# Optimization experiments

Measured on AMD Instinct MI355X. Metric: run time of the kernel, lower is better.

The kernel has to match this reference:

```python
import jax, jax.numpy as jnp
import numpy as np

DIM = 256   # feat channels (init dim)
K = 32      # top-k neighbors (init k)
EPS = 1e-12 # torch F.normalize eps


def setup_inputs() -> dict:
    key = jax.random.key(0)
    # channels = DIM feat + 64 pos-encoding channels
    feat_pos = jax.random.normal(key, (16, 320, 32, 32), dtype=jnp.float32)
    return {"feat_pos": feat_pos}


def reference(feat_pos):
    b, ct, h, w = feat_pos.shape
    n = h * w
    # (b, c_total, h, w) -> (b, n, c_total)
    x = feat_pos.reshape(b, ct, n).transpose(0, 2, 1)
    feat = x[:, :, :DIM]          # (b, n, c)
    pos = x[:, :, DIM:]           # (b, n, p)
    # L2-normalize pos (torch F.normalize semantics: divide by max(norm, eps))
    pos = pos / jnp.maximum(jnp.linalg.norm(pos, axis=-1, keepdims=True), EPS)
    # pairwise cosine similarity (b, n, n)
    sim = jnp.einsum('bnd,bmd->bnm', pos, pos)
    # top-k neighbors per token (sorted descending, same as torch.topk)
    topksim, topkid = jax.lax.top_k(sim, K)          # (b, n, k)
    bidx = jnp.arange(b)[:, None, None]
    topkfeat = feat[bidx, topkid]                    # (b, n, k, c)
    attn = jax.nn.softmax(topksim, axis=-1)          # (b, n, k)
    out = jnp.einsum('bnk,bnkc->bnc', attn, topkfeat)  # (b, n, c)
    return out.reshape(b, h, w, DIM).transpose(0, 3, 1, 2)  # (b, c, h, w)
```

## Files before the change

kernel.cpp:

```cpp
#include <hip/hip_runtime.h>
#include <math.h>

#define CT    320
#define NPTS  1024
#define DFEAT 256
#define DPOS  64
#define KSEL  32

__global__ void gnn_rnj(const float* __restrict__ in, float* __restrict__ rnjg) {
  const int b     = blockIdx.x;
  const int batch = b >> 2;
  const int j     = ((b & 3) << 8) + threadIdx.x;
  const float* __restrict__ pbase = in + (size_t)batch * CT * NPTS + (size_t)DFEAT * NPTS;
  float s = 0.f;
#pragma unroll 8
  for (int d = 0; d < DPOS; ++d) {
    const float x = pbase[(size_t)d * NPTS + j];
    s = fmaf(x, x, s);
  }
  rnjg[batch * NPTS + j] = 1.0f / fmaxf(sqrtf(s), 1e-12f);
}

#define AROWS 16
#define DCH   2
#define QSTEP 6.103515625e-05f
__global__ __launch_bounds__(256, 4) void gnn_sim_topk(const float* __restrict__ in,
                                                       const float* __restrict__ rnjg,
                                                       float2* __restrict__ pairs) {
  __shared__ float pi[DPOS * 20];
  __shared__ float rnjL[NPTS];
  __shared__ float jt[3][DCH * 1024];
  __shared__ float cand[AROWS][68];

  const int p     = blockIdx.x;
  const int batch = ((p & 7) << 1) | ((p >> 3) & 1);
  const int chunk = p >> 4;
  const int i0    = chunk * AROWS;
  const int tid   = threadIdx.x;
  const int w     = tid >> 6;
  const int lane  = tid & 63;

  const float* __restrict__ pbase = in + (size_t)batch * CT * NPTS + (size_t)DFEAT * NPTS;

  {
    const int i = tid & 15;
    const int d0 = tid >> 4;
#pragma unroll
    for (int pass = 0; pass < 4; ++pass) {
      const int d = pass * 16 + d0;
      pi[d * 20 + i] = pbase[(size_t)d * NPTS + i0 + i];
    }
  }
  *(float4*)&rnjL[tid * 4] = *(const float4*)&rnjg[batch * NPTS + tid * 4];

#define JSTAGE(buf, c)                                                           \
  do {                                                                           \
    const int dd_   = (w >> 1);                                                  \
    const int half_ = (w & 1);                                                   \
    const float* src_ = pbase + (size_t)((c) * DCH + dd_) * NPTS + half_ * 512 + lane * 4; \
    float* dst_ = &jt[buf][dd_ * 1024 + half_ * 512];                            \
    __builtin_amdgcn_global_load_lds(                                            \
        (const __attribute__((address_space(1))) void*)(src_),                   \
        (__attribute__((address_space(3))) void*)(dst_), 16, 0, 0);              \
    __builtin_amdgcn_global_load_lds(                                            \
        (const __attribute__((address_space(1))) void*)(src_ + 256),             \
        (__attribute__((address_space(3))) void*)(dst_ + 256), 16, 0, 0);        \
  } while (0)

  JSTAGE(0, 0);
  JSTAGE(1, 1);
  asm volatile("s_waitcnt vmcnt(2)" ::: "memory");
  __syncthreads();

  float acc[4][16];
#pragma unroll
  for (int r = 0; r < 4; ++r)
#pragma unroll
    for (int s = 0; s < 16; ++s) acc[r][s] = 0.f;

  int cur = 0;
  for (int c = 0; c < DPOS / DCH; ++c) {
#pragma unroll
    for (int dd = 0; dd < DCH; ++dd) {
      const int d = c * DCH + dd;
      const float4 pv4 = *(const float4*)&pi[d * 20 + w * 4];
      const float pr_[4] = {pv4.x, pv4.y, pv4.z, pv4.w};
      float4 jv[4];
#pragma unroll
      for (int u = 0; u < 4; ++u)
        jv[u] = *(const float4*)&jt[cur][dd * 1024 + u * 256 + lane * 4];
#pragma unroll
      for (int r = 0; r < 4; ++r) {
#pragma unroll
        for (int u = 0; u < 4; ++u) {
          acc[r][u*4+0] = fmaf(pr_[r], jv[u].x, acc[r][u*4+0]);
          acc[r][u*4+1] = fmaf(pr_[r], jv[u].y, acc[r][u*4+1]);
          acc[r][u*4+2] = fmaf(pr_[r], jv[u].z, acc[r][u*4+2]);
          acc[r][u*4+3] = fmaf(pr_[r], jv[u].w, acc[r][u*4+3]);
        }
      }
    }
    if (c < DPOS / DCH - 2) {
      const int nbuf = (cur + 2 >= 3) ? cur - 1 : cur + 2;
      JSTAGE(nbuf, c + 2);
      asm volatile("s_waitcnt vmcnt(2)" ::: "memory");
    } else {
      asm volatile("s_waitcnt vmcnt(0)" ::: "memory");
    }
    __syncthreads();
    cur = (cur + 1 >= 3) ? 0 : cur + 1;
  }
#undef JSTAGE

  float4 rv[4];
#pragma unroll
  for (int u = 0; u < 4; ++u) rv[u] = *(const float4*)&rnjL[u * 256 + lane * 4];

#pragma unroll
  for (int r = 0; r < 4; ++r) {
    const int rglob = w * 4 + r;
    const float sc = rnjL[i0 + rglob];
    float v[16];
#pragma unroll
    for (int u = 0; u < 4; ++u) {
      v[u*4+0] = acc[r][u*4+0] * rv[u].x * sc;
      v[u*4+1] = acc[r][u*4+1] * rv[u].y * sc;
      v[u*4+2] = acc[r][u*4+2] * rv[u].z * sc;
      v[u*4+3] = acc[r][u*4+3] * rv[u].w * sc;
    }
    int lo = 0;
#pragma unroll
    for (int bit = 16384; bit >= 1; bit >>= 1) {
      const float thrf = (float)(lo + bit) * QSTEP - 1.0f;
      int cnt = 0;
#pragma unroll
      for (int t = 0; t < 16; ++t) cnt += (int)__popcll(__ballot(v[t] >= thrf));
      if (cnt >= KSEL) lo += bit;
    }
    const float thr_h = (float)(lo + 1) * QSTEP - 1.0f;
    const float thr_l = (float)lo * QSTEP - 1.0f;
    int cbase = 0;
    unsigned cmask = 0u;
#pragma unroll
    for (int t = 0; t < 16; ++t) {
      const bool hi = (v[t] >= thr_h);
      const unsigned long long m = __ballot(hi);
      if (hi) {
        const int pos = cbase + (int)__builtin_amdgcn_mbcnt_hi(
            (unsigned)(m >> 32), __builtin_amdgcn_mbcnt_lo((unsigned)m, 0u));
        const int j = (t >> 2) * 256 + lane * 4 + (t & 3);
        *(float2*)&cand[rglob][2 * pos] = make_float2(v[t], __int_as_float(j));
      }
      cbase += (int)__popcll(m);
      if ((v[t] >= thr_l) && !hi) cmask |= (1u << t);
    }
    const int need = KSEL - cbase;
    for (int it = 0; it < need; ++it) {
      float bv = -2.0f; int bj = 0x7fffffff; int bt = 16;
#pragma unroll
      for (int t = 0; t < 16; ++t) {
        if (((cmask >> t) & 1u) && v[t] > bv) {
          bv = v[t]; bj = (t >> 2) * 256 + lane * 4 + (t & 3); bt = t;
        }
      }
      float rvv = bv; int rj = bj;
#pragma unroll
      for (int s = 1; s < 64; s <<= 1) {
        const float ov = __shfl_xor(rvv, s);
        const int   oj = __shfl_xor(rj, s);
        if (ov > rvv || (ov == rvv && oj < rj)) { rvv = ov; rj = oj; }
      }
      if (bv == rvv && bj == rj) {
        *(float2*)&cand[rglob][2 * (cbase + it)] = make_float2(bv, __int_as_float(bj));
        cmask &= ~(1u << bt);
      }
    }
    {
      const float x = cand[rglob][2 * (lane & 31)];
      float mx = x;
#pragma unroll
      for (int s = 16; s >= 1; s >>= 1) mx = fmaxf(mx, __shfl_xor(mx, s));
      const float e = expf(x - mx);
      float sum = e;
#pragma unroll
      for (int s = 16; s >= 1; s >>= 1) sum += __shfl_xor(sum, s);
      if (lane < KSEL) cand[rglob][2 * lane] = e / sum;
    }
  }
  __syncthreads();

  {
    const int pidx = tid * 2;
    const int r = pidx >> 5, k = pidx & 31;
    const float4 o4 = *(const float4*)&cand[r][2 * k];
    *(float4*)&pairs[((size_t)batch * NPTS + i0 + r) * KSEL + k] = o4;
  }
}

__global__ __launch_bounds__(256, 2) void gnn_gather(const float* __restrict__ in,
                                                     const float2* __restrict__ pairs,
                                                     float* __restrict__ out) {
  __shared__ float fst[4][4096];

  const int p     = blockIdx.x;
  const int batch = ((p & 7) << 1) | ((p >> 3) & 1);
  const int chunk = p >> 4;
  const int i0    = chunk * 32;
  const int tid   = threadIdx.x;
  const int w     = tid >> 6;
  const int lane  = tid & 63;
  const int row   = lane & 31;
  const int khalf = lane >> 5;
  const int ch0   = w * 64;

  const float* __restrict__ fbase = in + (size_t)batch * CT * NPTS;
  float* const fw = &fst[w][0];

  float a16[16]; int jjb[16];
  {
    const float4* pr4 = (const float4*)(pairs + ((size_t)batch * NPTS + i0 + row) * KSEL)
                        + khalf * 8;
#pragma unroll
    for (int qq = 0; qq < 8; ++qq) {
      const float4 o = pr4[qq];
      const int id0 = __float_as_int(o.y);
      const int id1 = __float_as_int(o.w);
      a16[2*qq]   = o.x;
      jjb[2*qq]   = ((((id0 & 3) << 6) | ((id0 >> 2) & 63) | (id0 & ~255)) << 4);
      a16[2*qq+1] = o.z;
      jjb[2*qq+1] = ((((id1 & 3) << 6) | ((id1 >> 2) & 63) | (id1 & ~255)) << 4);
    }
  }

  float4 tile[4][4];

#define LOADT(pp)                                                                \
  do {                                                                           \
    _Pragma("unroll")                                                            \
    for (int it = 0; it < 4; ++it) {                                             \
      _Pragma("unroll")                                                          \
      for (int c = 0; c < 4; ++c)                                                \
        tile[it][c] = *(const float4*)(fbase +                                   \
            (size_t)(ch0 + (pp) * 4 + c) * NPTS + it * 256 + lane * 4);          \
    }                                                                            \
  } while (0)

#define WRITET()                                                                 \
  do {                                                                           \
    _Pragma("unroll")                                                            \
    for (int it = 0; it < 4; ++it) {                                             \
      *(float4*)&fw[(256*it + lane) * 4] =                                       \
          make_float4(tile[it][0].x, tile[it][1].x, tile[it][2].x, tile[it][3].x);\
      *(float4*)&fw[(256*it + 64 + lane) * 4] =                                  \
          make_float4(tile[it][0].y, tile[it][1].y, tile[it][2].y, tile[it][3].y);\
      *(float4*)&fw[(256*it + 128 + lane) * 4] =                                 \
          make_float4(tile[it][0].z, tile[it][1].z, tile[it][2].z, tile[it][3].z);\
      *(float4*)&fw[(256*it + 192 + lane) * 4] =                                 \
          make_float4(tile[it][0].w, tile[it][1].w, tile[it][2].w, tile[it][3].w);\
    }                                                                            \
  } while (0)

  LOADT(0);
  WRITET();

  for (int pp = 0; pp < 16; ++pp) {
    if (pp < 15) LOADT(pp + 1);

    float4 o4 = make_float4(0.f, 0.f, 0.f, 0.f);
#pragma unroll
    for (int kk = 0; kk < 16; ++kk) {
      const float4 f4 = *(const float4*)((const char*)fw + jjb[kk]);
      const float ak = a16[kk];
      o4.x = fmaf(ak, f4.x, o4.x);
      o4.y = fmaf(ak, f4.y, o4.y);
      o4.z = fmaf(ak, f4.z, o4.z);
      o4.w = fmaf(ak, f4.w, o4.w);
    }
    o4.x += __shfl_xor(o4.x, 32);
    o4.y += __shfl_xor(o4.y, 32);
    o4.z += __shfl_xor(o4.z, 32);
    o4.w += __shfl_xor(o4.w, 32);

    float* ob = out + ((size_t)batch * DFEAT + ch0 + pp * 4) * NPTS + i0 + row;
    if (khalf == 0) {
      ob[0]            = o4.x;
      ob[(size_t)NPTS] = o4.y;
    } else {
      ob[(size_t)2 * NPTS] = o4.z;
      ob[(size_t)3 * NPTS] = o4.w;
    }

    if (pp < 15) WRITET();
  }
#undef LOADT
#undef WRITET
}

extern "C" void kernel_launch(void* const* d_in, const int* in_sizes, int n_in,
                              void* d_out, int out_size, void* d_ws, size_t ws_size,
                              hipStream_t stream) {
  const float* in = (const float*)d_in[0];
  float* out = (float*)d_out;
  float2* pairs = (float2*)d_ws;
  float*  rnjg  = (float*)((char*)d_ws + (16u << 20) / 4);
  gnn_rnj<<<dim3(64), dim3(256), 0, stream>>>(in, rnjg);
  gnn_sim_topk<<<dim3(1024), dim3(256), 0, stream>>>(in, rnjg, pairs);
  gnn_gather<<<dim3(512), dim3(256), 0, stream>>>(in, pairs, out);
}
```

Baseline: 98.92 us.

## Compute similarity with split-bf16 MFMA and two-stage per-wave top-k

A prep kernel now normalizes the position vectors and splits each value into three bf16 parts (hi, mid, lo), written row-major to workspace. The similarity kernel computes dot products with 16x16x32 bf16 MFMA over six cross-term products, which approximates fp32 accuracy, instead of FP32 FMAs through an LDS-staged pipeline. Top-k becomes two-stage: each wave picks 32 candidates from its own 256 columns, then a second threshold search merges the 128 candidates per row. This removes the scalar FMA bottleneck at the cost of extra prep traffic, a slight precision risk on near-tie selections, and lower occupancy (launch bound 2).

Measured after the change: 129.8 us. 1.31x slower.

```diff
diff --git a/kernel.cpp b/kernel.cpp
--- a/kernel.cpp
+++ b/kernel.cpp
@@ -6,177 +6,259 @@
 #define DFEAT 256
 #define DPOS  64
 #define KSEL  32
-
-__global__ void gnn_rnj(const float* __restrict__ in, float* __restrict__ rnjg) {
+#define QSTEP 6.103515625e-05f
+
+typedef __attribute__((ext_vector_type(8))) short short8;
+typedef __attribute__((ext_vector_type(4))) float f32x4;
+
+__device__ __forceinline__ unsigned bf16_rne(float x) {
+  const unsigned u = __float_as_uint(x);
+  return (u + 0x7FFFu + ((u >> 16) & 1u)) >> 16;
+}
+__device__ __forceinline__ float bf16_back(unsigned h) {
+  return __uint_as_float(h << 16);
+}
+
+__global__ __launch_bounds__(256) void gnn_phat(const float* __restrict__ in,
+                                                unsigned short* __restrict__ ph0,
+                                                unsigned short* __restrict__ ph1,
+                                                unsigned short* __restrict__ ph2) {
   const int b     = blockIdx.x;
   const int batch = b >> 2;
   const int j     = ((b & 3) << 8) + threadIdx.x;
   const float* __restrict__ pbase = in + (size_t)batch * CT * NPTS + (size_t)DFEAT * NPTS;
-  float s = 0.f;
-#pragma unroll 8
+
+  float x[DPOS];
+  float ssq = 0.f;
+#pragma unroll
   for (int d = 0; d < DPOS; ++d) {
-    const float x = pbase[(size_t)d * NPTS + j];
-    s = fmaf(x, x, s);
-  }
-  rnjg[batch * NPTS + j] = 1.0f / fmaxf(sqrtf(s), 1e-12f);
-}
-
-#define AROWS 16
-#define DCH   2
-#define QSTEP 6.103515625e-05f
-__global__ __launch_bounds__(256, 4) void gnn_sim_topk(const float* __restrict__ in,
-                                                       const float* __restrict__ rnjg,
+    x[d] = pbase[(size_t)d * NPTS + j];
+    ssq = fmaf(x[d], x[d], ssq);
+  }
+  const float rn = 1.0f / fmaxf(sqrtf(ssq), 1e-12f);
+
+  const size_t rowoff = ((size_t)batch * NPTS + j) * DPOS;
+  uint4* r0 = (uint4*)(ph0 + rowoff);
+  uint4* r1 = (uint4*)(ph1 + rowoff);
+  uint4* r2 = (uint4*)(ph2 + rowoff);
+#pragma unroll
+  for (int qd = 0; qd < 8; ++qd) {
+    unsigned a0[8], a1[8], a2[8];
+#pragma unroll
+    for (int e = 0; e < 8; ++e) {
+      const float y = x[qd * 8 + e] * rn;
+      a0[e] = bf16_rne(y);
+      const float s1 = y - bf16_back(a0[e]);
+      a1[e] = bf16_rne(s1);
+      const float s2 = s1 - bf16_back(a1[e]);
+      a2[e] = bf16_rne(s2);
+    }
+    uint4 v;
+    v.x = a0[0] | (a0[1] << 16); v.y = a0[2] | (a0[3] << 16);
+    v.z = a0[4] | (a0[5] << 16); v.w = a0[6] | (a0[7] << 16);
+    r0[qd] = v;
+    v.x = a1[0] | (a1[1] << 16); v.y = a1[2] | (a1[3] << 16);
+    v.z = a1[4] | (a1[5] << 16); v.w = a1[6] | (a1[7] << 16);
+    r1[qd] = v;
+    v.x = a2[0] | (a2[1] << 16); v.y = a2[2] | (a2[3] << 16);
+    v.z = a2[4] | (a2[5] << 16); v.w = a2[6] | (a2[7] << 16);
+    r2[qd] = v;
+  }
+}
+
+__global__ __launch_bounds__(256, 2) void gnn_sim_topk(const unsigned short* __restrict__ ph0,
+                                                       const unsigned short* __restrict__ ph1,
+                                                       const unsigned short* __restrict__ ph2,
                                                        float2* __restrict__ pairs) {
-  __shared__ float pi[DPOS * 20];
-  __shared__ float rnjL[NPTS];
-  __shared__ float jt[3][DCH * 1024];
-  __shared__ float cand[AROWS][68];
+  __shared__ float cand[16][260];
 
   const int p     = blockIdx.x;
   const int batch = ((p & 7) << 1) | ((p >> 3) & 1);
   const int chunk = p >> 4;
-  const int i0    = chunk * AROWS;
+  const int i0    = chunk * 16;
   const int tid   = threadIdx.x;
   const int w     = tid >> 6;
   const int lane  = tid & 63;
-
-  const float* __restrict__ pbase = in + (size_t)batch * CT * NPTS + (size_t)DFEAT * NPTS;
-
+  const int il    = lane & 15;
+  const int g     = lane >> 4;
+
+  const size_t bb = (size_t)batch * NPTS;
+
+  short8 bfr[2][3];
   {
-    const int i = tid & 15;
-    const int d0 = tid >> 4;
-#pragma unroll
-    for (int pass = 0; pass < 4; ++pass) {
-      const int d = pass * 16 + d0;
-      pi[d * 20 + i] = pbase[(size_t)d * NPTS + i0 + i];
-    }
-  }
-  *(float4*)&rnjL[tid * 4] = *(const float4*)&rnjg[batch * NPTS + tid * 4];
-
-#define JSTAGE(buf, c)                                                           \
-  do {                                                                           \
-    const int dd_   = (w >> 1);                                                  \
-    const int half_ = (w & 1);                                                   \
-    const float* src_ = pbase + (size_t)((c) * DCH + dd_) * NPTS + half_ * 512 + lane * 4; \
-    float* dst_ = &jt[buf][dd_ * 1024 + half_ * 512];                            \
-    __builtin_amdgcn_global_load_lds(                                            \
-        (const __attribute__((address_space(1))) void*)(src_),                   \
-        (__attribute__((address_space(3))) void*)(dst_), 16, 0, 0);              \
-    __builtin_amdgcn_global_load_lds(                                            \
-        (const __attribute__((address_space(1))) void*)(src_ + 256),             \
-        (__attribute__((address_space(3))) void*)(dst_ + 256), 16, 0, 0);        \
-  } while (0)
-
-  JSTAGE(0, 0);
-  JSTAGE(1, 1);
-  asm volatile("s_waitcnt vmcnt(2)" ::: "memory");
+    const size_t off = (bb + i0 + il) * DPOS + g * 8;
+#pragma unroll
+    for (int ks = 0; ks < 2; ++ks) {
+      bfr[ks][0] = *(const short8*)(ph0 + off + ks * 32);
+      bfr[ks][1] = *(const short8*)(ph1 + off + ks * 32);
+      bfr[ks][2] = *(const short8*)(ph2 + off + ks * 32);
+    }
+  }
+
+  f32x4 acc[16];
+#pragma unroll
+  for (int nt = 0; nt < 16; ++nt) acc[nt] = (f32x4){0.f, 0.f, 0.f, 0.f};
+
+  const size_t jo = (bb + w * 256 + il) * DPOS + g * 8;
+
+#pragma unroll
+  for (int ks = 0; ks < 2; ++ks) {
+    short8 afr[16];
+#pragma unroll
+    for (int nt = 0; nt < 16; ++nt)
+      afr[nt] = *(const short8*)(ph0 + jo + (size_t)nt * 16 * DPOS + ks * 32);
+#pragma unroll
+    for (int nt = 0; nt < 16; ++nt)
+      acc[nt] = __builtin_amdgcn_mfma_f32_16x16x32_bf16(afr[nt], bfr[ks][0], acc[nt], 0, 0, 0);
+#pragma unroll
+    for (int nt = 0; nt < 16; ++nt)
+      acc[nt] = __builtin_amdgcn_mfma_f32_16x16x32_bf16(afr[nt], bfr[ks][1], acc[nt], 0, 0, 0);
+#pragma unroll
+    for (int nt = 0; nt < 16; ++nt)
+      acc[nt] = __builtin_amdgcn_mfma_f32_16x16x32_bf16(afr[nt], bfr[ks][2], acc[nt], 0, 0, 0);
+#pragma unroll
+    for (int nt = 0; nt < 16; ++nt)
+      afr[nt] = *(const short8*)(ph1 + jo + (size_t)nt * 16 * DPOS + ks * 32);
+#pragma unroll
+    for (int nt = 0; nt < 16; ++nt)
+      acc[nt] = __builtin_amdgcn_mfma_f32_16x16x32_bf16(afr[nt], bfr[ks][0], acc[nt], 0, 0, 0);
+#pragma unroll
+    for (int nt = 0; nt < 16; ++nt)
+      acc[nt] = __builtin_amdgcn_mfma_f32_16x16x32_bf16(afr[nt], bfr[ks][1], acc[nt], 0, 0, 0);
+#pragma unroll
+    for (int nt = 0; nt < 16; ++nt)
+      afr[nt] = *(const short8*)(ph2 + jo + (size_t)nt * 16 * DPOS + ks * 32);
+#pragma unroll
+    for (int nt = 0; nt < 16; ++nt)
+      acc[nt] = __builtin_amdgcn_mfma_f32_16x16x32_bf16(afr[nt], bfr[ks][0], acc[nt], 0, 0, 0);
+  }
+
+  const int jb = w * 256 + g * 4;
+  int lo = 0;
+#pragma unroll
+  for (int bit = 16384; bit >= 1; bit >>= 1) {
+    const float thrf = (float)(lo + bit) * QSTEP - 1.0f;
+    int cnt = 0;
+#pragma unroll
+    for (int nt = 0; nt < 16; ++nt)
+#pragma unroll
+      for (int r = 0; r < 4; ++r) cnt += (acc[nt][r] >= thrf) ? 1 : 0;
+    const int c2 = cnt + __shfl_xor(cnt, 16);
+    const int c4 = c2 + __shfl_xor(c2, 32);
+    if (c4 >= KSEL) lo += bit;
+  }
+  const float thr_h = (float)(lo + 1) * QSTEP - 1.0f;
+  const float thr_l = (float)lo * QSTEP - 1.0f;
+
+  int lcnt = 0;
+#pragma unroll
+  for (int nt = 0; nt < 16; ++nt)
+#pragma unroll
+    for (int r = 0; r < 4; ++r) lcnt += (acc[nt][r] >= thr_h) ? 1 : 0;
+  const int cO = __shfl_xor(lcnt, 16);
+  const int cT = __shfl_xor(lcnt, 32);
+  const int cH = __shfl_xor(cO, 32);
+  const int cbase = lcnt + cO + cT + cH;
+  const int pre = (g == 0) ? 0 : (g == 1) ? cO : (g == 2) ? (cT + cH) : (cO + cT + cH);
+
+  {
+    int pos = pre;
+#pragma unroll
+    for (int nt = 0; nt < 16; ++nt) {
+#pragma unroll
+      for (int r = 0; r < 4; ++r) {
+        if (acc[nt][r] >= thr_h) {
+          *(float2*)&cand[il][2 * (w * KSEL + pos)] =
+              make_float2(acc[nt][r], __int_as_float(jb + nt * 16 + r));
+          ++pos;
+        }
+      }
+    }
+  }
+  unsigned long long bm = 0ull;
+#pragma unroll
+  for (int nt = 0; nt < 16; ++nt)
+#pragma unroll
+    for (int r = 0; r < 4; ++r)
+      if (acc[nt][r] >= thr_l && acc[nt][r] < thr_h) bm |= (1ull << (nt * 4 + r));
+  const int need = KSEL - cbase;
+  for (int it = 0; it < need; ++it) {
+    float bv = -2.0f; int bj = 0x7fffffff; int bs = 0;
+#pragma unroll
+    for (int nt = 0; nt < 16; ++nt) {
+#pragma unroll
+      for (int r = 0; r < 4; ++r) {
+        if (((bm >> (nt * 4 + r)) & 1ull) && acc[nt][r] > bv) {
+          bv = acc[nt][r]; bj = jb + nt * 16 + r; bs = nt * 4 + r;
+        }
+      }
+    }
+    float rv = bv; int rj = bj;
+    {
+      const float ov = __shfl_xor(rv, 16); const int oj = __shfl_xor(rj, 16);
+      if (ov > rv || (ov == rv && oj < rj)) { rv = ov; rj = oj; }
+    }
+    {
+      const float ov = __shfl_xor(rv, 32); const int oj = __shfl_xor(rj, 32);
+      if (ov > rv || (ov == rv && oj < rj)) { rv = ov; rj = oj; }
+    }
+    if (bv == rv && bj == rj) {
+      *(float2*)&cand[il][2 * (w * KSEL + cbase + it)] = make_float2(bv, __int_as_float(bj));
+      bm &= ~(1ull << bs);
+    }
+  }
   __syncthreads();
 
-  float acc[4][16];
-#pragma unroll
-  for (int r = 0; r < 4; ++r)
-#pragma unroll
-    for (int s = 0; s < 16; ++s) acc[r][s] = 0.f;
-
-  int cur = 0;
-  for (int c = 0; c < DPOS / DCH; ++c) {
-#pragma unroll
-    for (int dd = 0; dd < DCH; ++dd) {
-      const int d = c * DCH + dd;
-      const float4 pv4 = *(const float4*)&pi[d * 20 + w * 4];
-      const float pr_[4] = {pv4.x, pv4.y, pv4.z, pv4.w};
-      float4 jv[4];
-#pragma unroll
-      for (int u = 0; u < 4; ++u)
-        jv[u] = *(const float4*)&jt[cur][dd * 1024 + u * 256 + lane * 4];
-#pragma unroll
-      for (int r = 0; r < 4; ++r) {
-#pragma unroll
-        for (int u = 0; u < 4; ++u) {
-          acc[r][u*4+0] = fmaf(pr_[r], jv[u].x, acc[r][u*4+0]);
-          acc[r][u*4+1] = fmaf(pr_[r], jv[u].y, acc[r][u*4+1]);
-          acc[r][u*4+2] = fmaf(pr_[r], jv[u].z, acc[r][u*4+2]);
-          acc[r][u*4+3] = fmaf(pr_[r], jv[u].w, acc[r][u*4+3]);
-        }
-      }
-    }
-    if (c < DPOS / DCH - 2) {
-      const int nbuf = (cur + 2 >= 3) ? cur - 1 : cur + 2;
-      JSTAGE(nbuf, c + 2);
-      asm volatile("s_waitcnt vmcnt(2)" ::: "memory");
-    } else {
-      asm volatile("s_waitcnt vmcnt(0)" ::: "memory");
-    }
-    __syncthreads();
-    cur = (cur + 1 >= 3) ? 0 : cur + 1;
-  }
-#undef JSTAGE
-
-  float4 rv[4];
-#pragma unroll
-  for (int u = 0; u < 4; ++u) rv[u] = *(const float4*)&rnjL[u * 256 + lane * 4];
-
-#pragma unroll
-  for (int r = 0; r < 4; ++r) {
-    const int rglob = w * 4 + r;
-    const float sc = rnjL[i0 + rglob];
-    float v[16];
-#pragma unroll
-    for (int u = 0; u < 4; ++u) {
-      v[u*4+0] = acc[r][u*4+0] * rv[u].x * sc;
-      v[u*4+1] = acc[r][u*4+1] * rv[u].y * sc;
-      v[u*4+2] = acc[r][u*4+2] * rv[u].z * sc;
-      v[u*4+3] = acc[r][u*4+3] * rv[u].w * sc;
-    }
-    int lo = 0;
+#pragma unroll
+  for (int rr = 0; rr < 4; ++rr) {
+    const int r = w * 4 + rr;
+    const float4 c4 = *(const float4*)&cand[r][lane * 4];
+    float v2[2] = { c4.x, c4.z };
+    int   j2[2] = { __float_as_int(c4.y), __float_as_int(c4.w) };
+    int lo2 = 0;
 #pragma unroll
     for (int bit = 16384; bit >= 1; bit >>= 1) {
-      const float thrf = (float)(lo + bit) * QSTEP - 1.0f;
-      int cnt = 0;
-#pragma unroll
-      for (int t = 0; t < 16; ++t) cnt += (int)__popcll(__ballot(v[t] >= thrf));
-      if (cnt >= KSEL) lo += bit;
-    }
-    const float thr_h = (float)(lo + 1) * QSTEP - 1.0f;
-    const float thr_l = (float)lo * QSTEP - 1.0f;
-    int cbase = 0;
-    unsigned cmask = 0u;
-#pragma unroll
-    for (int t = 0; t < 16; ++t) {
-      const bool hi = (v[t] >= thr_h);
+      const float thrf = (float)(lo2 + bit) * QSTEP - 1.0f;
+      const int cnt = (int)__popcll(__ballot(v2[0] >= thrf)) +
+                      (int)__popcll(__ballot(v2[1] >= thrf));
+      if (cnt >= KSEL) lo2 += bit;
+    }
+    const float th = (float)(lo2 + 1) * QSTEP - 1.0f;
+    const float tl = (float)lo2 * QSTEP - 1.0f;
+    int cb = 0; unsigned cm = 0u;
+#pragma unroll
+    for (int t = 0; t < 2; ++t) {
+      const bool hi = (v2[t] >= th);
       const unsigned long long m = __ballot(hi);
       if (hi) {
-        const int pos = cbase + (int)__builtin_amdgcn_mbcnt_hi(
+        const int ps = cb + (int)__builtin_amdgcn_mbcnt_hi(
             (unsigned)(m >> 32), __builtin_amdgcn_mbcnt_lo((unsigned)m, 0u));
-        const int j = (t >> 2) * 256 + lane * 4 + (t & 3);
-        *(float2*)&cand[rglob][2 * pos] = make_float2(v[t], __int_as_float(j));
-      }
-      cbase += (int)__popcll(m);
-      if ((v[t] >= thr_l) && !hi) cmask |= (1u << t);
-    }
-    const int need = KSEL - cbase;
-    for (int it = 0; it < need; ++it) {
-      float bv = -2.0f; int bj = 0x7fffffff; int bt = 16;
-#pragma unroll
-      for (int t = 0; t < 16; ++t) {
-        if (((cmask >> t) & 1u) && v[t] > bv) {
-          bv = v[t]; bj = (t >> 2) * 256 + lane * 4 + (t & 3); bt = t;
-        }
-      }
-      float rvv = bv; int rj = bj;
+        *(float2*)&cand[r][2 * ps] = make_float2(v2[t], __int_as_float(j2[t]));
+      }
+      cb += (int)__popcll(m);
+      if (v2[t] >= tl && !hi) cm |= (1u << t);
+    }
+    const int nd = KSEL - cb;
+    for (int it = 0; it < nd; ++it) {
+      float bv = -2.0f; int bj = 0x7fffffff; int bt = 2;
+#pragma unroll
+      for (int t = 0; t < 2; ++t) {
+        if (((cm >> t) & 1u) && v2[t] > bv) { bv = v2[t]; bj = j2[t]; bt = t; }
+      }
+      float rv = bv; int rj = bj;
 #pragma unroll
       for (int s = 1; s < 64; s <<= 1) {
-        const float ov = __shfl_xor(rvv, s);
+        const float ov = __shfl_xor(rv, s);
         const int   oj = __shfl_xor(rj, s);
-        if (ov > rvv || (ov == rvv && oj < rj)) { rvv = ov; rj = oj; }
-      }
-      if (bv == rvv && bj == rj) {
-        *(float2*)&cand[rglob][2 * (cbase + it)] = make_float2(bv, __int_as_float(bj));
-        cmask &= ~(1u << bt);
+        if (ov > rv || (ov == rv && oj < rj)) { rv = ov; rj = oj; }
+      }
+      if (bv == rv && bj == rj) {
+        *(float2*)&cand[r][2 * (cb + it)] = make_float2(bv, __int_as_float(bj));
+        cm &= ~(1u << bt);
       }
     }
     {
-      const float x = cand[rglob][2 * (lane & 31)];
+      const float x = cand[r][2 * (lane & 31)];
       float mx = x;
 #pragma unroll
       for (int s = 16; s >= 1; s >>= 1) mx = fmaxf(mx, __shfl_xor(mx, s));
@@ -184,7 +266,7 @@
       float sum = e;
 #pragma unroll
       for (int s = 16; s >= 1; s >>= 1) sum += __shfl_xor(sum, s);
-      if (lane < KSEL) cand[rglob][2 * lane] = e / sum;
+      if (lane < KSEL) cand[r][2 * lane] = e / sum;
     }
   }
   __syncthreads();
@@ -302,8 +384,10 @@
   const float* in = (const float*)d_in[0];
   float* out = (float*)d_out;
   float2* pairs = (float2*)d_ws;
-  float*  rnjg  = (float*)((char*)d_ws + (16u << 20) / 4);
-  gnn_rnj<<<dim3(64), dim3(256), 0, stream>>>(in, rnjg);
-  gnn_sim_topk<<<dim3(1024), dim3(256), 0, stream>>>(in, rnjg, pairs);
+  unsigned short* ph0 = (unsigned short*)((char*)d_ws + (4u << 20));
+  unsigned short* ph1 = (unsigned short*)((char*)d_ws + (6u << 20));
+  unsigned short* ph2 = (unsigned short*)((char*)d_ws + (8u << 20));
+  gnn_phat<<<dim3(64), dim3(256), 0, stream>>>(in, ph0, ph1, ph2);
+  gnn_sim_topk<<<dim3(1024), dim3(256), 0, stream>>>(ph0, ph1, ph2, pairs);
   gnn_gather<<<dim3(512), dim3(256), 0, stream>>>(in, pairs, out);
 }
```

## Retile gather kernel so each block handles 64 rows over half the channels

Applied to the files above, without the earlier changes.

Each gather block now covers 64 output rows and 128 channels instead of 32 rows and all 256 channels. Every staged feature tile in shared memory is therefore reused by two row groups, which halves the global feature reloads per output row. Each thread holds two sets of neighbor weights and indices, which raises register pressure against the launch bounds of two blocks per SM.

Result: faster. 94.19 us (median of 2 runs) (-4.8%).

```diff
diff --git a/kernel.cpp b/kernel.cpp
--- a/kernel.cpp
+++ b/kernel.cpp
@@ -205,30 +205,35 @@
   const int p     = blockIdx.x;
   const int batch = ((p & 7) << 1) | ((p >> 3) & 1);
   const int chunk = p >> 4;
-  const int i0    = chunk * 32;
+  const int rchk  = chunk >> 1;
+  const int chalf = chunk & 1;
+  const int i0    = rchk * 64;
   const int tid   = threadIdx.x;
   const int w     = tid >> 6;
   const int lane  = tid & 63;
-  const int row   = lane & 31;
+  const int rs    = lane & 31;
   const int khalf = lane >> 5;
-  const int ch0   = w * 64;
+  const int ch0   = chalf * 128 + w * 32;
 
   const float* __restrict__ fbase = in + (size_t)batch * CT * NPTS;
   float* const fw = &fst[w][0];
 
-  float a16[16]; int jjb[16];
+  float aA[16], aB[16]; int jA[16], jB[16];
   {
-    const float4* pr4 = (const float4*)(pairs + ((size_t)batch * NPTS + i0 + row) * KSEL)
+    const float4* prA = (const float4*)(pairs + ((size_t)batch * NPTS + i0 + rs) * KSEL)
                         + khalf * 8;
+    const float4* prB = (const float4*)(pairs + ((size_t)batch * NPTS + i0 + 32 + rs) * KSEL)
+                        + khalf * 8;
 #pragma unroll
     for (int qq = 0; qq < 8; ++qq) {
-      const float4 o = pr4[qq];
-      const int id0 = __float_as_int(o.y);
-      const int id1 = __float_as_int(o.w);
-      a16[2*qq]   = o.x;
-      jjb[2*qq]   = ((((id0 & 3) << 6) | ((id0 >> 2) & 63) | (id0 & ~255)) << 4);
-      a16[2*qq+1] = o.z;
-      jjb[2*qq+1] = ((((id1 & 3) << 6) | ((id1 >> 2) & 63) | (id1 & ~255)) << 4);
+      const float4 oA = prA[qq];
+      const float4 oB = prB[qq];
+      const int a0 = __float_as_int(oA.y), a1 = __float_as_int(oA.w);
+      const int b0 = __float_as_int(oB.y), b1 = __float_as_int(oB.w);
+      aA[2*qq]   = oA.x; jA[2*qq]   = ((((a0 & 3) << 6) | ((a0 >> 2) & 63) | (a0 & ~255)) << 4);
+      aA[2*qq+1] = oA.z; jA[2*qq+1] = ((((a1 & 3) << 6) | ((a1 >> 2) & 63) | (a1 & ~255)) << 4);
+      aB[2*qq]   = oB.x; jB[2*qq]   = ((((b0 & 3) << 6) | ((b0 >> 2) & 63) | (b0 & ~255)) << 4);
+      aB[2*qq+1] = oB.z; jB[2*qq+1] = ((((b1 & 3) << 6) | ((b1 >> 2) & 63) | (b1 & ~255)) << 4);
     }
   }
 
@@ -263,34 +268,53 @@
   LOADT(0);
   WRITET();
 
-  for (int pp = 0; pp < 16; ++pp) {
-    if (pp < 15) LOADT(pp + 1);
-
-    float4 o4 = make_float4(0.f, 0.f, 0.f, 0.f);
+  for (int pp = 0; pp < 8; ++pp) {
+    if (pp < 7) LOADT(pp + 1);
+
+    float4 oA4 = make_float4(0.f, 0.f, 0.f, 0.f);
+    float4 oB4 = make_float4(0.f, 0.f, 0.f, 0.f);
 #pragma unroll
     for (int kk = 0; kk < 16; ++kk) {
-      const float4 f4 = *(const float4*)((const char*)fw + jjb[kk]);
-      const float ak = a16[kk];
-      o4.x = fmaf(ak, f4.x, o4.x);
-      o4.y = fmaf(ak, f4.y, o4.y);
-      o4.z = fmaf(ak, f4.z, o4.z);
-      o4.w = fmaf(ak, f4.w, o4.w);
-    }
-    o4.x += __shfl_xor(o4.x, 32);
-    o4.y += __shfl_xor(o4.y, 32);
-    o4.z += __shfl_xor(o4.z, 32);
-    o4.w += __shfl_xor(o4.w, 32);
-
-    float* ob = out + ((size_t)batch * DFEAT + ch0 + pp * 4) * NPTS + i0 + row;
+      const float4 fA = *(const float4*)((const char*)fw + jA[kk]);
+      const float ak = aA[kk];
+      oA4.x = fmaf(ak, fA.x, oA4.x);
+      oA4.y = fmaf(ak, fA.y, oA4.y);
+      oA4.z = fmaf(ak, fA.z, oA4.z);
+      oA4.w = fmaf(ak, fA.w, oA4.w);
+    }
+#pragma unroll
+    for (int kk = 0; kk < 16; ++kk) {
+      const float4 fB = *(const float4*)((const char*)fw + jB[kk]);
+      const float bk = aB[kk];
+      oB4.x = fmaf(bk, fB.x, oB4.x);
+      oB4.y = fmaf(bk, fB.y, oB4.y);
+      oB4.z = fmaf(bk, fB.z, oB4.z);
+      oB4.w = fmaf(bk, fB.w, oB4.w);
+    }
+    oA4.x += __shfl_xor(oA4.x, 32);
+    oA4.y += __shfl_xor(oA4.y, 32);
+    oA4.z += __shfl_xor(oA4.z, 32);
+    oA4.w += __shfl_xor(oA4.w, 32);
+    oB4.x += __shfl_xor(oB4.x, 32);
+    oB4.y += __shfl_xor(oB4.y, 32);
+    oB4.z += __shfl_xor(oB4.z, 32);
+    oB4.w += __shfl_xor(oB4.w, 32);
+
+    float* obA = out + ((size_t)batch * DFEAT + ch0 + pp * 4) * NPTS + i0 + rs;
+    float* obB = obA + 32;
     if (khalf == 0) {
-      ob[0]            = o4.x;
-      ob[(size_t)NPTS] = o4.y;
+      obA[0]            = oA4.x;
+      obA[(size_t)NPTS] = oA4.y;
+      obB[0]            = oB4.x;
+      obB[(size_t)NPTS] = oB4.y;
     } else {
-      ob[(size_t)2 * NPTS] = o4.z;
-      ob[(size_t)3 * NPTS] = o4.w;
-    }
-
-    if (pp < 15) WRITET();
+      obA[(size_t)2 * NPTS] = oA4.z;
+      obA[(size_t)3 * NPTS] = oA4.w;
+      obB[(size_t)2 * NPTS] = oB4.z;
+      obB[(size_t)3 * NPTS] = oB4.w;
+    }
+
+    if (pp < 7) WRITET();
   }
 #undef LOADT
 #undef WRITET
```

## Retile gather kernel so each block covers 128 rows and a 64-channel quarter

Applied to the files above, without the earlier changes.

The gather kernel's work split changes: each block now handles 128 query rows over 64 channels (16 per wave) instead of 32 rows over all 256 channels. Each channel tile staged in shared memory is reused by four row groups, so the per-block feature reload drops from all 256 channels to 64 across the grid. The cost is four sets of neighbor indices and weights held in registers per thread, which adds register pressure and may reduce occupancy. Pair data is now read four times per row (once per channel quarter) instead of once.

Measured after the change: 160.1 us. 61.8% more time.

```diff
diff --git a/kernel.cpp b/kernel.cpp
--- a/kernel.cpp
+++ b/kernel.cpp
@@ -205,32 +205,40 @@
   const int p     = blockIdx.x;
   const int batch = ((p & 7) << 1) | ((p >> 3) & 1);
   const int chunk = p >> 4;
-  const int i0    = chunk * 32;
+  const int rchk  = chunk >> 2;
+  const int cq    = chunk & 3;
+  const int i0    = rchk * 128;
   const int tid   = threadIdx.x;
   const int w     = tid >> 6;
   const int lane  = tid & 63;
-  const int row   = lane & 31;
+  const int rs    = lane & 31;
   const int khalf = lane >> 5;
-  const int ch0   = w * 64;
+  const int ch0   = cq * 64 + w * 16;
 
   const float* __restrict__ fbase = in + (size_t)batch * CT * NPTS;
   float* const fw = &fst[w][0];
 
-  float a16[16]; int jjb[16];
-  {
-    const float4* pr4 = (const float4*)(pairs + ((size_t)batch * NPTS + i0 + row) * KSEL)
-                        + khalf * 8;
-#pragma unroll
-    for (int qq = 0; qq < 8; ++qq) {
-      const float4 o = pr4[qq];
-      const int id0 = __float_as_int(o.y);
-      const int id1 = __float_as_int(o.w);
-      a16[2*qq]   = o.x;
-      jjb[2*qq]   = ((((id0 & 3) << 6) | ((id0 >> 2) & 63) | (id0 & ~255)) << 4);
-      a16[2*qq+1] = o.z;
-      jjb[2*qq+1] = ((((id1 & 3) << 6) | ((id1 >> 2) & 63) | (id1 & ~255)) << 4);
-    }
-  }
+  float aA[16], aB[16], aC[16], aD[16];
+  int   jA[16], jB[16], jC[16], jD[16];
+#define LDPAIRS(arr_a, arr_j, roff)                                              \
+  do {                                                                           \
+    const float4* pr4 = (const float4*)(pairs +                                  \
+        ((size_t)batch * NPTS + i0 + (roff) + rs) * KSEL) + khalf * 8;           \
+    _Pragma("unroll")                                                            \
+    for (int qq = 0; qq < 8; ++qq) {                                             \
+      const float4 o = pr4[qq];                                                  \
+      const int d0 = __float_as_int(o.y), d1 = __float_as_int(o.w);              \
+      arr_a[2*qq]   = o.x;                                                       \
+      arr_j[2*qq]   = ((((d0 & 3) << 6) | ((d0 >> 2) & 63) | (d0 & ~255)) << 4); \
+      arr_a[2*qq+1] = o.z;                                                       \
+      arr_j[2*qq+1] = ((((d1 & 3) << 6) | ((d1 >> 2) & 63) | (d1 & ~255)) << 4); \
+    }                                                                            \
+  } while (0)
+  LDPAIRS(aA, jA, 0);
+  LDPAIRS(aB, jB, 32);
+  LDPAIRS(aC, jC, 64);
+  LDPAIRS(aD, jD, 96);
+#undef LDPAIRS
 
   float4 tile[4][4];
 
@@ -260,40 +268,56 @@
     }                                                                            \
   } while (0)
 
+#define GATHER(arr_a, arr_j, ovar)                                               \
+  do {                                                                           \
+    _Pragma("unroll")                                                            \
+    for (int kk = 0; kk < 16; ++kk) {                                            \
+      const float4 f4 = *(const float4*)((const char*)fw + arr_j[kk]);           \
+      const float ak = arr_a[kk];                                                \
+      ovar.x = fmaf(ak, f4.x, ovar.x);                                           \
+      ovar.y = fmaf(ak, f4.y, ovar.y);                                           \
+      ovar.z = fmaf(ak, f4.z, ovar.z);                                           \
+      ovar.w = fmaf(ak, f4.w, ovar.w);                                           \
+    }                                                                            \
+    ovar.x += __shfl_xor(ovar.x, 32);                                            \
+    ovar.y += __shfl_xor(ovar.y, 32);                                            \
+    ovar.z += __shfl_xor(ovar.z, 32);                                            \
+    ovar.w += __shfl_xor(ovar.w, 32);                                            \
+  } while (0)
+
   LOADT(0);
   WRITET();
 
-  for (int pp = 0; pp < 16; ++pp) {
-    if (pp < 15) LOADT(pp + 1);
-
-    float4 o4 = make_float4(0.f, 0.f, 0.f, 0.f);
-#pragma unroll
-    for (int kk = 0; kk < 16; ++kk) {
-      const float4 f4 = *(const float4*)((const char*)fw + jjb[kk]);
-      const float ak = a16[kk];
-      o4.x = fmaf(ak, f4.x, o4.x);
-      o4.y = fmaf(ak, f4.y, o4.y);
-      o4.z = fmaf(ak, f4.z, o4.z);
-      o4.w = fmaf(ak, f4.w, o4.w);
-    }
-    o4.x += __shfl_xor(o4.x, 32);
-    o4.y += __shfl_xor(o4.y, 32);
-    o4.z += __shfl_xor(o4.z, 32);
-    o4.w += __shfl_xor(o4.w, 32);
-
-    float* ob = out + ((size_t)batch * DFEAT + ch0 + pp * 4) * NPTS + i0 + row;
+  for (int pp = 0; pp < 4; ++pp) {
+    if (pp < 3) LOADT(pp + 1);
+
+    float4 oA = make_float4(0.f, 0.f, 0.f, 0.f);
+    float4 oB = make_float4(0.f, 0.f, 0.f, 0.f);
+    float4 oC = make_float4(0.f, 0.f, 0.f, 0.f);
+    float4 oD = make_float4(0.f, 0.f, 0.f, 0.f);
+    GATHER(aA, jA, oA);
+    GATHER(aB, jB, oB);
+    GATHER(aC, jC, oC);
+    GATHER(aD, jD, oD);
+
+    float* ob = out + ((size_t)batch * DFEAT + ch0 + pp * 4) * NPTS + i0 + rs;
     if (khalf == 0) {
-      ob[0]            = o4.x;
-      ob[(size_t)NPTS] = o4.y;
+      ob[0]   = oA.x;  ob[(size_t)NPTS]      = oA.y;
+      ob[32]  = oB.x;  ob[(size_t)NPTS + 32] = oB.y;
+      ob[64]  = oC.x;  ob[(size_t)NPTS + 64] = oC.y;
+      ob[96]  = oD.x;  ob[(size_t)NPTS + 96] = oD.y;
     } else {
-      ob[(size_t)2 * NPTS] = o4.z;
-      ob[(size_t)3 * NPTS] = o4.w;
-    }
-
-    if (pp < 15) WRITET();
+      ob[(size_t)2 * NPTS]      = oA.z;  ob[(size_t)3 * NPTS]      = oA.w;
+      ob[(size_t)2 * NPTS + 32] = oB.z;  ob[(size_t)3 * NPTS + 32] = oB.w;
+      ob[(size_t)2 * NPTS + 64] = oC.z;  ob[(size_t)3 * NPTS + 64] = oC.w;
+      ob[(size_t)2 * NPTS + 96] = oD.z;  ob[(size_t)3 * NPTS + 96] = oD.w;
+    }
+
+    if (pp < 3) WRITET();
   }
 #undef LOADT
 #undef WRITET
+#undef GATHER
 }
 
 extern "C" void kernel_launch(void* const* d_in, const int* in_sizes, int n_in,
```
